# Optimization experiments

Hardware: AMD Instinct MI355X
Metric: run time of the kernel (lower is better)

Reference implementation:

```python
import jax, jax.numpy as jnp
import numpy as np

DT = 1.0 / 24000.0  # module default dt
Q_DECAY = 0.9       # refractory decay used in brf_dynamics

B, D = 4096, 4096


def setup_inputs() -> dict:
    key = jax.random.key(0)
    ks = jax.random.split(key, 7)
    x = jax.random.normal(ks[0], (B, D), dtype=jnp.float32)
    u = jax.random.normal(ks[1], (B, D), dtype=jnp.float32) * 0.1
    v = jax.random.normal(ks[2], (B, D), dtype=jnp.float32) * 0.1
    q = jax.random.uniform(ks[3], (B, D), dtype=jnp.float32)
    # per-neuron angular frequencies in ~[0, 1000] rad/s (dt*omega << 1)
    omegas = jax.random.uniform(ks[4], (D,), dtype=jnp.float32) * 1000.0
    bs = jax.random.uniform(ks[5], (D,), dtype=jnp.float32)
    threshold = jax.random.uniform(ks[6], (D,), dtype=jnp.float32)
    return {"x": x, "u": u, "v": v, "q": q,
            "omegas": omegas, "bs": bs, "threshold": threshold}


def _spike(s):
    # forward of StepDoubleGaussianGrad: Heaviside step
    return (s > 0).astype(s.dtype)


def reference(x, u, v, q, omegas, bs, threshold):
    omega = jnp.abs(omegas)                                   # [D]
    # sustain_osc: divergence boundary of the RF oscillator
    p_omega = (-1.0 + jnp.sqrt(1.0 - jnp.square(DT * omega))) / DT  # [D]
    b = p_omega - jnp.abs(bs) - q                             # [B, D]
    # brf_dynamics (note: v update uses the OLD u, as in the source)
    u_ = u + b * u * DT - omega * v * DT + x * DT
    v_new = v + omega * u * DT + b * v * DT
    z = _spike(jnp.abs(u_) - jnp.abs(threshold) - q)
    q_new = q * Q_DECAY + z
    return (z, u_, v_new, q_new)
```

## Files before the change

kernel.cpp:

```cpp
#include <hip/hip_runtime.h>
#include <math.h>


#define DTF ((float)(1.0 / 24000.0))
#define QDECAY 0.9f

__global__ void brf_coef_kernel(const float* __restrict__ omegas,
                                const float* __restrict__ bs,
                                const float* __restrict__ threshold,
                                float* __restrict__ coef, int D) {
#pragma clang fp contract(off)
    int i = blockIdx.x * blockDim.x + threadIdx.x;
    if (i < D) {
        float om = fabsf(omegas[i]);
        float t  = DTF * om;
        float s  = sqrtf(1.0f - t * t);
        float p  = (-1.0f + s) / DTF;
        coef[i]          = om;
        coef[D + i]      = p - fabsf(bs[i]);
        coef[2 * D + i]  = fabsf(threshold[i]);
    }
}

__device__ __forceinline__ void brf_elem(float x, float u, float v, float q,
                                         float om, float pw, float th,
                                         float& z, float& u_, float& vn, float& qn) {
#pragma clang fp contract(off)
    float b  = pw - q;
    float t1 = (b * u) * DTF;
    float t2 = (om * v) * DTF;
    float t3 = x * DTF;
    u_ = ((u + t1) - t2) + t3;
    float t4 = (om * u) * DTF;
    float t5 = (b * v) * DTF;
    vn = (v + t4) + t5;
    float s = (fabsf(u_) - th) - q;
    z  = (s > 0.0f) ? 1.0f : 0.0f;
    qn = q * QDECAY + z;
}

__global__ __launch_bounds__(256) void brf_main_kernel(
        const float4* __restrict__ x, const float4* __restrict__ u,
        const float4* __restrict__ v, const float4* __restrict__ q,
        const float* __restrict__ coef, float* __restrict__ out,
        int N4, int D4, int D) {
#pragma clang fp contract(off)
    const float4* omv = (const float4*)(coef);
    const float4* pwv = (const float4*)(coef + D);
    const float4* thv = (const float4*)(coef + 2 * D);
    float4* out_z = (float4*)out;
    float4* out_u = out_z + N4;
    float4* out_v = out_z + 2 * (size_t)N4;
    float4* out_q = out_z + 3 * (size_t)N4;

    const bool pow2 = (D4 & (D4 - 1)) == 0;
    int stride = gridDim.x * blockDim.x;
    for (int i = blockIdx.x * blockDim.x + threadIdx.x; i < N4; i += stride) {
        int c4 = pow2 ? (i & (D4 - 1)) : (i % D4);
        float4 xv = x[i], uv = u[i], vv = v[i], qv = q[i];
        float4 oc = omv[c4], pc = pwv[c4], tc = thv[c4];

        float4 rz, ru, rv, rq;
        brf_elem(xv.x, uv.x, vv.x, qv.x, oc.x, pc.x, tc.x, rz.x, ru.x, rv.x, rq.x);
        brf_elem(xv.y, uv.y, vv.y, qv.y, oc.y, pc.y, tc.y, rz.y, ru.y, rv.y, rq.y);
        brf_elem(xv.z, uv.z, vv.z, qv.z, oc.z, pc.z, tc.z, rz.z, ru.z, rv.z, rq.z);
        brf_elem(xv.w, uv.w, vv.w, qv.w, oc.w, pc.w, tc.w, rz.w, ru.w, rv.w, rq.w);

        out_z[i] = rz;
        out_u[i] = ru;
        out_v[i] = rv;
        out_q[i] = rq;
    }
}

extern "C" void kernel_launch(void* const* d_in, const int* in_sizes, int n_in,
                              void* d_out, int out_size, void* d_ws, size_t ws_size,
                              hipStream_t stream) {
    const float* x   = (const float*)d_in[0];
    const float* u   = (const float*)d_in[1];
    const float* v   = (const float*)d_in[2];
    const float* q   = (const float*)d_in[3];
    const float* om  = (const float*)d_in[4];
    const float* bs  = (const float*)d_in[5];
    const float* th  = (const float*)d_in[6];
    float* out = (float*)d_out;
    float* coef = (float*)d_ws;

    int N = in_sizes[0];
    int D = in_sizes[4];
    int N4 = N / 4;
    int D4 = D / 4;

    brf_coef_kernel<<<(D + 255) / 256, 256, 0, stream>>>(om, bs, th, coef, D);

    int blocks = (N4 + 255) / 256;
    if (blocks > 2048) blocks = 2048;
    brf_main_kernel<<<blocks, 256, 0, stream>>>(
        (const float4*)x, (const float4*)u, (const float4*)v, (const float4*)q,
        coef, out, N4, D4, D);
}
```

Measured before the change: 122.0 us.

## Fuse coefficient precompute into main kernel and use nontemporal loads/stores

Removes the separate coefficient kernel and computes per-column omega, damping and threshold coefficients inside the main kernel. The grid is rounded so that the grid stride is a multiple of the column count, which keeps each thread on a fixed column and lets it compute coefficients once. Streaming inputs and outputs use nontemporal loads and stores to reduce cache pollution. This saves a launch and the coefficient workspace traffic, but the grid rounding could change occupancy for other shapes.

```diff
diff --git a/kernel.cpp b/kernel.cpp
--- a/kernel.cpp
+++ b/kernel.cpp
@@ -5,22 +5,7 @@
 #define DTF ((float)(1.0 / 24000.0))
 #define QDECAY 0.9f
 
-__global__ void brf_coef_kernel(const float* __restrict__ omegas,
-                                const float* __restrict__ bs,
-                                const float* __restrict__ threshold,
-                                float* __restrict__ coef, int D) {
-#pragma clang fp contract(off)
-    int i = blockIdx.x * blockDim.x + threadIdx.x;
-    if (i < D) {
-        float om = fabsf(omegas[i]);
-        float t  = DTF * om;
-        float s  = sqrtf(1.0f - t * t);
-        float p  = (-1.0f + s) / DTF;
-        coef[i]          = om;
-        coef[D + i]      = p - fabsf(bs[i]);
-        coef[2 * D + i]  = fabsf(threshold[i]);
-    }
-}
+typedef float f32x4 __attribute__((ext_vector_type(4)));
 
 __device__ __forceinline__ void brf_elem(float x, float u, float v, float q,
                                          float om, float pw, float th,
@@ -39,37 +24,57 @@
     qn = q * QDECAY + z;
 }
 
-__global__ __launch_bounds__(256) void brf_main_kernel(
-        const float4* __restrict__ x, const float4* __restrict__ u,
-        const float4* __restrict__ v, const float4* __restrict__ q,
-        const float* __restrict__ coef, float* __restrict__ out,
-        int N4, int D4, int D) {
+__global__ __launch_bounds__(256) void brf_fused_kernel(
+        const f32x4* __restrict__ x, const f32x4* __restrict__ u,
+        const f32x4* __restrict__ v, const f32x4* __restrict__ q,
+        const float* __restrict__ omegas, const float* __restrict__ bs,
+        const float* __restrict__ threshold, float* __restrict__ out,
+        int N4, int D4) {
 #pragma clang fp contract(off)
-    const float4* omv = (const float4*)(coef);
-    const float4* pwv = (const float4*)(coef + D);
-    const float4* thv = (const float4*)(coef + 2 * D);
-    float4* out_z = (float4*)out;
-    float4* out_u = out_z + N4;
-    float4* out_v = out_z + 2 * (size_t)N4;
-    float4* out_q = out_z + 3 * (size_t)N4;
+    f32x4* out_z = (f32x4*)out;
+    f32x4* out_u = out_z + (size_t)N4;
+    f32x4* out_v = out_z + 2 * (size_t)N4;
+    f32x4* out_q = out_z + 3 * (size_t)N4;
 
-    const bool pow2 = (D4 & (D4 - 1)) == 0;
-    int stride = gridDim.x * blockDim.x;
-    for (int i = blockIdx.x * blockDim.x + threadIdx.x; i < N4; i += stride) {
-        int c4 = pow2 ? (i & (D4 - 1)) : (i % D4);
-        float4 xv = x[i], uv = u[i], vv = v[i], qv = q[i];
-        float4 oc = omv[c4], pc = pwv[c4], tc = thv[c4];
+    const int tid    = blockIdx.x * blockDim.x + threadIdx.x;
+    const int stride = gridDim.x * blockDim.x;
+    const int c4     = tid % D4;
 
-        float4 rz, ru, rv, rq;
-        brf_elem(xv.x, uv.x, vv.x, qv.x, oc.x, pc.x, tc.x, rz.x, ru.x, rv.x, rq.x);
-        brf_elem(xv.y, uv.y, vv.y, qv.y, oc.y, pc.y, tc.y, rz.y, ru.y, rv.y, rq.y);
-        brf_elem(xv.z, uv.z, vv.z, qv.z, oc.z, pc.z, tc.z, rz.z, ru.z, rv.z, rq.z);
-        brf_elem(xv.w, uv.w, vv.w, qv.w, oc.w, pc.w, tc.w, rz.w, ru.w, rv.w, rq.w);
+    f32x4 o4 = ((const f32x4*)omegas)[c4];
+    f32x4 b4 = ((const f32x4*)bs)[c4];
+    f32x4 h4 = ((const f32x4*)threshold)[c4];
+    float oc[4], pw[4], tc[4];
+#pragma unroll
+    for (int k = 0; k < 4; ++k) {
+        float om = fabsf(o4[k]);
+        float t  = DTF * om;
+        float tt = t * t;
+        float s  = sqrtf(1.0f - tt);
+        float p  = (-1.0f + s) / DTF;
+        oc[k] = om;
+        pw[k] = p - fabsf(b4[k]);
+        tc[k] = fabsf(h4[k]);
+    }
 
-        out_z[i] = rz;
-        out_u[i] = ru;
-        out_v[i] = rv;
-        out_q[i] = rq;
+    for (int i = tid; i < N4; i += stride) {
+        f32x4 xv = __builtin_nontemporal_load(&x[i]);
+        f32x4 uv = __builtin_nontemporal_load(&u[i]);
+        f32x4 vv = __builtin_nontemporal_load(&v[i]);
+        f32x4 qv = __builtin_nontemporal_load(&q[i]);
+
+        f32x4 rz, ru, rv, rq;
+#pragma unroll
+        for (int k = 0; k < 4; ++k) {
+            float z, u_, vn, qn;
+            brf_elem(xv[k], uv[k], vv[k], qv[k], oc[k], pw[k], tc[k],
+                     z, u_, vn, qn);
+            rz[k] = z; ru[k] = u_; rv[k] = vn; rq[k] = qn;
+        }
+
+        __builtin_nontemporal_store(rz, &out_z[i]);
+        __builtin_nontemporal_store(ru, &out_u[i]);
+        __builtin_nontemporal_store(rv, &out_v[i]);
+        __builtin_nontemporal_store(rq, &out_q[i]);
     }
 }
 
@@ -84,18 +89,22 @@
     const float* bs  = (const float*)d_in[5];
     const float* th  = (const float*)d_in[6];
     float* out = (float*)d_out;
-    float* coef = (float*)d_ws;
 
-    int N = in_sizes[0];
-    int D = in_sizes[4];
+    int N  = in_sizes[0];
+    int D  = in_sizes[4];
     int N4 = N / 4;
     int D4 = D / 4;
 
-    brf_coef_kernel<<<(D + 255) / 256, 256, 0, stream>>>(om, bs, th, coef, D);
-
     int blocks = (N4 + 255) / 256;
     if (blocks > 2048) blocks = 2048;
-    brf_main_kernel<<<blocks, 256, 0, stream>>>(
-        (const float4*)x, (const float4*)u, (const float4*)v, (const float4*)q,
-        coef, out, N4, D4, D);
+    {
+        int g = 256, b = D4;
+        while (b) { int t = g % b; g = b; b = t; }
+        int m = D4 / g;
+        blocks = ((blocks + m - 1) / m) * m;
+    }
+
+    brf_fused_kernel<<<blocks, 256, 0, stream>>>(
+        (const f32x4*)x, (const f32x4*)u, (const f32x4*)v, (const f32x4*)q,
+        om, bs, th, out, N4, D4);
 }
```

Result: faster. 103.4 us (-15.3%).

## Restructure main kernel into per-wave burst loads with nontemporal memory ops

Applied to the files above, without the earlier changes.

Replaces the grid-stride loop with a non-looping kernel where each wave handles a contiguous run of 512 float4s, issuing all 32 vector loads up front, then computing, then issuing all stores. Loads and stores use nontemporal builtins to skip cache retention for streaming data, and the grid is sized to cover the full problem. This aims to raise memory-level parallelism on a purely bandwidth-bound elementwise kernel, at the cost of higher register pressure and a tail path for partial runs.

```diff
diff --git a/kernel.cpp b/kernel.cpp
--- a/kernel.cpp
+++ b/kernel.cpp
@@ -4,6 +4,8 @@
 
 #define DTF ((float)(1.0 / 24000.0))
 #define QDECAY 0.9f
+
+typedef float f32x4 __attribute__((ext_vector_type(4)));
 
 __global__ void brf_coef_kernel(const float* __restrict__ omegas,
                                 const float* __restrict__ bs,
@@ -14,7 +16,8 @@
     if (i < D) {
         float om = fabsf(omegas[i]);
         float t  = DTF * om;
-        float s  = sqrtf(1.0f - t * t);
+        float tt = t * t;
+        float s  = sqrtf(1.0f - tt);
         float p  = (-1.0f + s) / DTF;
         coef[i]          = om;
         coef[D + i]      = p - fabsf(bs[i]);
@@ -39,37 +42,90 @@
     qn = q * QDECAY + z;
 }
 
-__global__ __launch_bounds__(256) void brf_main_kernel(
-        const float4* __restrict__ x, const float4* __restrict__ u,
-        const float4* __restrict__ v, const float4* __restrict__ q,
+#define RUN 512
+#define TG  4
+
+__global__ __launch_bounds__(256) void brf_burst_kernel(
+        const f32x4* __restrict__ x, const f32x4* __restrict__ u,
+        const f32x4* __restrict__ v, const f32x4* __restrict__ q,
         const float* __restrict__ coef, float* __restrict__ out,
         int N4, int D4, int D) {
 #pragma clang fp contract(off)
-    const float4* omv = (const float4*)(coef);
-    const float4* pwv = (const float4*)(coef + D);
-    const float4* thv = (const float4*)(coef + 2 * D);
-    float4* out_z = (float4*)out;
-    float4* out_u = out_z + N4;
-    float4* out_v = out_z + 2 * (size_t)N4;
-    float4* out_q = out_z + 3 * (size_t)N4;
+    const f32x4* omv = (const f32x4*)(coef);
+    const f32x4* pwv = (const f32x4*)(coef + D);
+    const f32x4* thv = (const f32x4*)(coef + 2 * D);
+    f32x4* out_z = (f32x4*)out;
+    f32x4* out_u = out_z + (size_t)N4;
+    f32x4* out_v = out_z + 2 * (size_t)N4;
+    f32x4* out_q = out_z + 3 * (size_t)N4;
 
+    const int tid  = blockIdx.x * blockDim.x + threadIdx.x;
+    const int lane = tid & 63;
+    const int wave = tid >> 6;
+    const int base = wave * RUN + lane;
     const bool pow2 = (D4 & (D4 - 1)) == 0;
-    int stride = gridDim.x * blockDim.x;
-    for (int i = blockIdx.x * blockDim.x + threadIdx.x; i < N4; i += stride) {
-        int c4 = pow2 ? (i & (D4 - 1)) : (i % D4);
-        float4 xv = x[i], uv = u[i], vv = v[i], qv = q[i];
-        float4 oc = omv[c4], pc = pwv[c4], tc = thv[c4];
 
-        float4 rz, ru, rv, rq;
-        brf_elem(xv.x, uv.x, vv.x, qv.x, oc.x, pc.x, tc.x, rz.x, ru.x, rv.x, rq.x);
-        brf_elem(xv.y, uv.y, vv.y, qv.y, oc.y, pc.y, tc.y, rz.y, ru.y, rv.y, rq.y);
-        brf_elem(xv.z, uv.z, vv.z, qv.z, oc.z, pc.z, tc.z, rz.z, ru.z, rv.z, rq.z);
-        brf_elem(xv.w, uv.w, vv.w, qv.w, oc.w, pc.w, tc.w, rz.w, ru.w, rv.w, rq.w);
+    if (base + (RUN - 64) < N4) {
+        f32x4 X[8], U[8], V[8], Q[8];
+#pragma unroll
+        for (int t = 0; t < TG; ++t) X[t] = __builtin_nontemporal_load(&x[base + t * 64]);
+#pragma unroll
+        for (int t = 0; t < TG; ++t) U[t] = __builtin_nontemporal_load(&u[base + t * 64]);
+#pragma unroll
+        for (int t = 0; t < TG; ++t) V[t] = __builtin_nontemporal_load(&v[base + t * 64]);
+#pragma unroll
+        for (int t = 0; t < TG; ++t) Q[t] = __builtin_nontemporal_load(&q[base + t * 64]);
+#pragma unroll
+        for (int t = TG; t < 8; ++t) X[t] = __builtin_nontemporal_load(&x[base + t * 64]);
+#pragma unroll
+        for (int t = TG; t < 8; ++t) U[t] = __builtin_nontemporal_load(&u[base + t * 64]);
+#pragma unroll
+        for (int t = TG; t < 8; ++t) V[t] = __builtin_nontemporal_load(&v[base + t * 64]);
+#pragma unroll
+        for (int t = TG; t < 8; ++t) Q[t] = __builtin_nontemporal_load(&q[base + t * 64]);
 
-        out_z[i] = rz;
-        out_u[i] = ru;
-        out_v[i] = rv;
-        out_q[i] = rq;
+        f32x4 RZ[8], RU[8], RV[8], RQ[8];
+#pragma unroll
+        for (int t = 0; t < 8; ++t) {
+            int idx = base + t * 64;
+            int c4  = pow2 ? (idx & (D4 - 1)) : (idx % D4);
+            f32x4 oc = omv[c4], pc = pwv[c4], tc = thv[c4];
+#pragma unroll
+            for (int k = 0; k < 4; ++k) {
+                float z, u_, vn, qn;
+                brf_elem(X[t][k], U[t][k], V[t][k], Q[t][k],
+                         oc[k], pc[k], tc[k], z, u_, vn, qn);
+                RZ[t][k] = z; RU[t][k] = u_; RV[t][k] = vn; RQ[t][k] = qn;
+            }
+        }
+
+#pragma unroll
+        for (int t = 0; t < 8; ++t) __builtin_nontemporal_store(RZ[t], &out_z[base + t * 64]);
+#pragma unroll
+        for (int t = 0; t < 8; ++t) __builtin_nontemporal_store(RU[t], &out_u[base + t * 64]);
+#pragma unroll
+        for (int t = 0; t < 8; ++t) __builtin_nontemporal_store(RV[t], &out_v[base + t * 64]);
+#pragma unroll
+        for (int t = 0; t < 8; ++t) __builtin_nontemporal_store(RQ[t], &out_q[base + t * 64]);
+    } else {
+#pragma unroll
+        for (int t = 0; t < 8; ++t) {
+            int i = base + t * 64;
+            if (i < N4) {
+                int c4 = pow2 ? (i & (D4 - 1)) : (i % D4);
+                f32x4 xv = x[i], uv = u[i], vv = v[i], qv = q[i];
+                f32x4 oc = omv[c4], pc = pwv[c4], tc = thv[c4];
+                f32x4 rz, ru, rv, rq;
+#pragma unroll
+                for (int k = 0; k < 4; ++k) {
+                    float z, u_, vn, qn;
+                    brf_elem(xv[k], uv[k], vv[k], qv[k], oc[k], pc[k], tc[k],
+                             z, u_, vn, qn);
+                    rz[k] = z; ru[k] = u_; rv[k] = vn; rq[k] = qn;
+                }
+                out_z[i] = rz; out_u[i] = ru; out_v[i] = rv; out_q[i] = rq;
+            }
+        }
     }
 }
 
@@ -83,19 +139,19 @@
     const float* om  = (const float*)d_in[4];
     const float* bs  = (const float*)d_in[5];
     const float* th  = (const float*)d_in[6];
-    float* out = (float*)d_out;
+    float* out  = (float*)d_out;
     float* coef = (float*)d_ws;
 
-    int N = in_sizes[0];
-    int D = in_sizes[4];
+    int N  = in_sizes[0];
+    int D  = in_sizes[4];
     int N4 = N / 4;
     int D4 = D / 4;
 
     brf_coef_kernel<<<(D + 255) / 256, 256, 0, stream>>>(om, bs, th, coef, D);
 
-    int blocks = (N4 + 255) / 256;
-    if (blocks > 2048) blocks = 2048;
-    brf_main_kernel<<<blocks, 256, 0, stream>>>(
-        (const float4*)x, (const float4*)u, (const float4*)v, (const float4*)q,
+    int waves  = (N4 + RUN - 1) / RUN;
+    int blocks = (waves + 3) / 4;
+    brf_burst_kernel<<<blocks, 256, 0, stream>>>(
+        (const f32x4*)x, (const f32x4*)u, (const f32x4*)v, (const f32x4*)q,
         coef, out, N4, D4, D);
 }
```

Result: faster. 107.6 us (-11.8%).
